# Optimization experiments

Hardware: AMD Instinct MI355X
Metric: run time of the kernel (lower is better)

Reference implementation:

```python
import jax, jax.numpy as jnp
import numpy as np

# NuclearLossFunc: loss = trace(sum_bc A_bc^T A_bc) / (B*C)
# trace(A^T A) == sum of squared elements of A, so the bmm is mathematically
# equivalent to a single elementwise-square-and-sum reduction.

def setup_inputs() -> dict:
    key = jax.random.key(0)
    inputs = jax.random.normal(key, (32, 64, 256, 256), dtype=jnp.float32)
    return {"inputs": inputs}

def reference(inputs) -> jnp.ndarray:
    B, C, Sx, Sy = inputs.shape
    # trace(sum_{b,c} A^T A) = sum over all elements squared
    loss = jnp.sum(jnp.square(inputs)) / (B * C)
    return loss
```

## Files before the change

### kernel.cpp

```cpp
#include <hip/hip_runtime.h>


__global__ __launch_bounds__(256) void nuclear_loss_kernel(
    const float4* __restrict__ in, float* __restrict__ out,
    long long n4, float scale)
{
    long long idx    = (long long)blockIdx.x * blockDim.x + threadIdx.x;
    long long stride = (long long)gridDim.x * blockDim.x;

    float acc = 0.0f;
    for (long long i = idx; i < n4; i += stride) {
        float4 v = in[i];
        acc += v.x * v.x + v.y * v.y + v.z * v.z + v.w * v.w;
    }

    #pragma unroll
    for (int off = 32; off > 0; off >>= 1)
        acc += __shfl_down(acc, off, 64);

    __shared__ float smem[4];
    int lane = threadIdx.x & 63;
    int wave = threadIdx.x >> 6;
    if (lane == 0) smem[wave] = acc;
    __syncthreads();

    if (threadIdx.x == 0) {
        float s = smem[0] + smem[1] + smem[2] + smem[3];
        atomicAdd(out, s * scale);
    }
}

extern "C" void kernel_launch(void* const* d_in, const int* in_sizes, int n_in,
                              void* d_out, int out_size, void* d_ws, size_t ws_size,
                              hipStream_t stream) {
    const float* in = (const float*)d_in[0];
    float* out = (float*)d_out;

    long long n  = (long long)in_sizes[0];
    long long n4 = n / 4;
    const float scale = 1.0f / 2048.0f;

    hipMemsetAsync(d_out, 0, (size_t)out_size * sizeof(float), stream);

    const int block = 256;
    const int grid  = 8192;
    nuclear_loss_kernel<<<grid, block, 0, stream>>>(
        (const float4*)in, out, n4, scale);
}
```

Measured before the change: 694.1 us.

## Unroll loads 4x and replace atomic accumulation with two-pass reduction

The streaming loop now issues four independent float4 loads per iteration into separate accumulators, which raises memory-level parallelism. Each block writes its partial sum to workspace instead of doing an atomicAdd, and a second single-block kernel reduces the partials and applies the scale. The grid shrinks from 8192 to 2048 blocks and the memset is dropped. The cost is an extra kernel launch and a dependence on the workspace size.

```diff
diff --git a/kernel.cpp b/kernel.cpp
--- a/kernel.cpp
+++ b/kernel.cpp
@@ -1,18 +1,29 @@
 #include <hip/hip_runtime.h>
 
 
-__global__ __launch_bounds__(256) void nuclear_loss_kernel(
-    const float4* __restrict__ in, float* __restrict__ out,
-    long long n4, float scale)
+__global__ __launch_bounds__(256) void nl_partial(
+    const float4* __restrict__ in, float* __restrict__ partial, long long n4)
 {
     long long idx    = (long long)blockIdx.x * blockDim.x + threadIdx.x;
     long long stride = (long long)gridDim.x * blockDim.x;
 
-    float acc = 0.0f;
-    for (long long i = idx; i < n4; i += stride) {
+    float a0 = 0.f, a1 = 0.f, a2 = 0.f, a3 = 0.f;
+    long long i = idx;
+    for (; i + 3 * stride < n4; i += 4 * stride) {
+        float4 v0 = in[i];
+        float4 v1 = in[i + stride];
+        float4 v2 = in[i + 2 * stride];
+        float4 v3 = in[i + 3 * stride];
+        a0 += v0.x * v0.x + v0.y * v0.y + v0.z * v0.z + v0.w * v0.w;
+        a1 += v1.x * v1.x + v1.y * v1.y + v1.z * v1.z + v1.w * v1.w;
+        a2 += v2.x * v2.x + v2.y * v2.y + v2.z * v2.z + v2.w * v2.w;
+        a3 += v3.x * v3.x + v3.y * v3.y + v3.z * v3.z + v3.w * v3.w;
+    }
+    for (; i < n4; i += stride) {
         float4 v = in[i];
-        acc += v.x * v.x + v.y * v.y + v.z * v.z + v.w * v.w;
+        a0 += v.x * v.x + v.y * v.y + v.z * v.z + v.w * v.w;
     }
+    float acc = (a0 + a1) + (a2 + a3);
 
     #pragma unroll
     for (int off = 32; off > 0; off >>= 1)
@@ -24,10 +35,30 @@
     if (lane == 0) smem[wave] = acc;
     __syncthreads();
 
-    if (threadIdx.x == 0) {
-        float s = smem[0] + smem[1] + smem[2] + smem[3];
-        atomicAdd(out, s * scale);
-    }
+    if (threadIdx.x == 0)
+        partial[blockIdx.x] = smem[0] + smem[1] + smem[2] + smem[3];
+}
+
+__global__ __launch_bounds__(256) void nl_final(
+    const float* __restrict__ partial, float* __restrict__ out,
+    int nparts, float scale)
+{
+    float acc = 0.f;
+    for (int i = threadIdx.x; i < nparts; i += 256)
+        acc += partial[i];
+
+    #pragma unroll
+    for (int off = 32; off > 0; off >>= 1)
+        acc += __shfl_down(acc, off, 64);
+
+    __shared__ float smem[4];
+    int lane = threadIdx.x & 63;
+    int wave = threadIdx.x >> 6;
+    if (lane == 0) smem[wave] = acc;
+    __syncthreads();
+
+    if (threadIdx.x == 0)
+        out[0] = (smem[0] + smem[1] + smem[2] + smem[3]) * scale;
 }
 
 extern "C" void kernel_launch(void* const* d_in, const int* in_sizes, int n_in,
@@ -35,15 +66,15 @@
                               hipStream_t stream) {
     const float* in = (const float*)d_in[0];
     float* out = (float*)d_out;
+    float* partial = (float*)d_ws;
 
     long long n  = (long long)in_sizes[0];
     long long n4 = n / 4;
     const float scale = 1.0f / 2048.0f;
 
-    hipMemsetAsync(d_out, 0, (size_t)out_size * sizeof(float), stream);
+    const int block = 256;
+    const int grid  = 2048;
 
-    const int block = 256;
-    const int grid  = 8192;
-    nuclear_loss_kernel<<<grid, block, 0, stream>>>(
-        (const float4*)in, out, n4, scale);
+    nl_partial<<<grid, block, 0, stream>>>((const float4*)in, partial, n4);
+    nl_final<<<1, block, 0, stream>>>(partial, out, grid, scale);
 }
```

Measured after the change: 678.4 us. 2.3% less time.
